# Kernel tuning notes

Hardware: AMD Instinct MI355X
Metric: run time of the kernel (lower is better)

## Reference

```python
import jax, jax.numpy as jnp
import numpy as np

HIDDEN = 1024
N_HEADS = 16
N_KV = 4
HEAD_DIM = HIDDEN // N_HEADS  # 64


def setup_inputs() -> dict:
    key = jax.random.key(0)
    ks = jax.random.split(key, 10)
    B, S, D = 2, 2048, HIDDEN
    s = 0.02
    return {
        "hidden_states": jax.random.normal(ks[0], (B, S, D), jnp.float32),
        "attention_mask": jnp.ones((B, S), jnp.float32),
        "Wq": jax.random.normal(ks[1], (D, N_HEADS * HEAD_DIM), jnp.float32) * s,
        "bq": jnp.zeros((N_HEADS * HEAD_DIM,), jnp.float32),
        "Wk": jax.random.normal(ks[2], (D, N_KV * HEAD_DIM), jnp.float32) * s,
        "bk": jnp.zeros((N_KV * HEAD_DIM,), jnp.float32),
        "Wv": jax.random.normal(ks[3], (D, N_KV * HEAD_DIM), jnp.float32) * s,
        "bv": jnp.zeros((N_KV * HEAD_DIM,), jnp.float32),
        "Wo": jax.random.normal(ks[4], (D, D), jnp.float32) * s,
        "bo": jnp.zeros((D,), jnp.float32),
    }


def _rope(x):
    # x: [B, H, S, Dh]; half-split RoPE as in the torch module
    S, Dh = x.shape[-2], x.shape[-1]
    inv_freq = 1.0 / (10000.0 ** (jnp.arange(0, Dh, 2, dtype=jnp.float32) / Dh))
    freqs = jnp.arange(S, dtype=jnp.float32)[:, None] * inv_freq[None, :]  # [S, Dh/2]
    cos, sin = jnp.cos(freqs), jnp.sin(freqs)
    x1, x2 = jnp.split(x, 2, axis=-1)
    return jnp.concatenate([x1 * cos - x2 * sin, x1 * sin + x2 * cos], axis=-1)


def reference(hidden_states, attention_mask, Wq, bq, Wk, bk, Wv, bv, Wo, bo):
    B, S, D = hidden_states.shape
    q = (hidden_states @ Wq + bq).reshape(B, S, N_HEADS, HEAD_DIM).transpose(0, 2, 1, 3)
    k = (hidden_states @ Wk + bk).reshape(B, S, N_KV, HEAD_DIM).transpose(0, 2, 1, 3)
    v = (hidden_states @ Wv + bv).reshape(B, S, N_KV, HEAD_DIM).transpose(0, 2, 1, 3)
    q = _rope(q)
    k = _rope(k)
    rep = N_HEADS // N_KV
    k = jnp.repeat(k, rep, axis=1)  # [B, H, S, Dh]
    v = jnp.repeat(v, rep, axis=1)
    bias = (1.0 - attention_mask[:, None, None, :]) * -1e9  # [B,1,1,S]
    scores = jnp.einsum("bhqd,bhkd->bhqk", q, k) / jnp.sqrt(jnp.float32(HEAD_DIM))
    attn = jax.nn.softmax(scores + bias, axis=-1)
    out = jnp.einsum("bhqk,bhkd->bhqd", attn, v)
    out = out.transpose(0, 2, 1, 3).reshape(B, S, D)
    return out @ Wo + bo
```

## Files before the change

kernel.cpp:

```cpp
#include <hip/hip_runtime.h>

typedef __bf16 bf16;
typedef __attribute__((ext_vector_type(8))) __bf16 bf16x8;
typedef __attribute__((ext_vector_type(4))) __bf16 bf16x4;
typedef __attribute__((ext_vector_type(4))) float f32x4;
typedef __attribute__((ext_vector_type(16))) float f32x16;
typedef __attribute__((ext_vector_type(4))) unsigned int uint4v;

#define LOG2E 1.44269504088896340736f
#define QSCALE 0.18033688011112042f

__device__ inline void tr_tile(const float* __restrict__ in, bf16* __restrict__ out,
                               int R, int C, int bx, int by, int tid) {
    __shared__ float t[32][33];
    int tx = tid & 31, ty = tid >> 5;
    int rbase = by * 32, cbase = bx * 32;
#pragma unroll
    for (int i = 0; i < 4; i++) {
        int r = ty + i * 8;
        t[r][tx] = in[(size_t)(rbase + r) * C + cbase + tx];
    }
    __syncthreads();
#pragma unroll
    for (int i = 0; i < 4; i++) {
        int r = ty + i * 8;
        out[(size_t)(cbase + r) * R + rbase + tx] = (bf16)t[tx][r];
    }
}

__global__ __launch_bounds__(256) void prep_k(const float* __restrict__ X,
                                              const float* __restrict__ Wq,
                                              const float* __restrict__ Wk,
                                              const float* __restrict__ Wv,
                                              const float* __restrict__ Wo,
                                              const float* __restrict__ mask,
                                              bf16* __restrict__ Xb,
                                              bf16* __restrict__ WqT,
                                              bf16* __restrict__ WkT,
                                              bf16* __restrict__ WvT,
                                              bf16* __restrict__ WoT,
                                              float2* __restrict__ rt,
                                              float* __restrict__ Mb,
                                              int* __restrict__ mflags) {
    int blk = blockIdx.x, tid = threadIdx.x;
    if (blk < 2048) {
        int idx = (blk * 256 + tid) * 8;
        float4 a = *(const float4*)(X + idx);
        float4 b = *(const float4*)(X + idx + 4);
        bf16 v[8] = {(bf16)a.x, (bf16)a.y, (bf16)a.z, (bf16)a.w,
                     (bf16)b.x, (bf16)b.y, (bf16)b.z, (bf16)b.w};
        *(uint4*)(Xb + idx) = *(const uint4*)v;
    } else if (blk < 3072) {
        int t = blk - 2048; tr_tile(Wq, WqT, 1024, 1024, t & 31, t >> 5, tid);
    } else if (blk < 3328) {
        int t = blk - 3072; tr_tile(Wk, WkT, 1024, 256, t & 7, t >> 3, tid);
    } else if (blk < 3584) {
        int t = blk - 3328; tr_tile(Wv, WvT, 1024, 256, t & 7, t >> 3, tid);
    } else if (blk < 4608) {
        int t = blk - 3584; tr_tile(Wo, WoT, 1024, 1024, t & 31, t >> 5, tid);
    } else if (blk < 4864) {
        int idx = (blk - 4608) * 256 + tid;
        int s = idx >> 5, i = idx & 31;
        float inv = exp2f(-0.41524100370589830f * (float)i);
        float ang = (float)s * inv;
        rt[idx] = make_float2(cosf(ang), sinf(ang));
    } else {
        __shared__ int sflag;
        int b = blk - 4864;
        if (tid == 0) sflag = 1;
        __syncthreads();
        const float* mrow = mask + (size_t)b * 2048;
        int i0 = tid * 8;
        bool ones = true;
#pragma unroll
        for (int j = 0; j < 8; j++) {
            float m = mrow[i0 + j];
            if (m != 1.0f) ones = false;
            Mb[(size_t)b * 2048 + i0 + j] = (1.0f - m) * (-1e9f) * LOG2E;
        }
        if (!ones) sflag = 0;
        __syncthreads();
        if (tid == 0) mflags[b] = sflag;
    }
}

__device__ __forceinline__ void gemm_main_db(bf16* __restrict__ pool,
                                             const bf16* __restrict__ A,
                                             const bf16* __restrict__ BT,
                                             int m0, int n0, int tid,
                                             f32x4 (&acc)[2][4]) {
    int w = tid >> 6, lane = tid & 63, l15 = lane & 15, quad = lane >> 4;

    int srow = lane >> 3;
    int kx = ((lane & 7) ^ srow) * 8;
    const bf16* ga0 = A + (size_t)(m0 + w * 32 + srow) * 1024 + kx;
    const bf16* gb0 = BT + (size_t)(n0 + w * 16 + srow) * 1024 + kx;
    int laofs = (w * 32) * 64 + lane * 8;
    int lbofs = 128 * 64 + (w * 16) * 64 + lane * 8;

#define GSTAGE(K0, BUF)                                                                             \
    do {                                                                                            \
        bf16* gbase = pool + (BUF) * 12288;                                                         \
        _Pragma("unroll")                                                                           \
        for (int p = 0; p < 4; p++)                                                                 \
            __builtin_amdgcn_global_load_lds(                                                       \
                (const __attribute__((address_space(1))) unsigned int*)(ga0 + (size_t)p * 8 * 1024 + (K0)), \
                (__attribute__((address_space(3))) unsigned int*)(gbase + laofs + p * 512), 16, 0, 0); \
        _Pragma("unroll")                                                                           \
        for (int p = 0; p < 2; p++)                                                                 \
            __builtin_amdgcn_global_load_lds(                                                       \
                (const __attribute__((address_space(1))) unsigned int*)(gb0 + (size_t)p * 8 * 1024 + (K0)), \
                (__attribute__((address_space(3))) unsigned int*)(gbase + lbofs + p * 512), 16, 0, 0); \
    } while (0)

    GSTAGE(0, 0);
    __syncthreads();

    for (int ks = 0; ks < 16; ks++) {
        int cb = ks & 1;
        if (ks < 15) GSTAGE((ks + 1) * 64, cb ^ 1);
        const bf16* As = pool + cb * 12288;
        const bf16* Bs = As + 128 * 64;
#pragma unroll
        for (int half = 0; half < 2; half++) {
            bf16x8 a[2], bfr[4];
            int kp = ((half * 4 + quad) ^ (l15 & 7)) * 8;
#pragma unroll
            for (int i = 0; i < 2; i++)
                a[i] = *(const bf16x8*)&As[(w * 32 + i * 16 + l15) * 64 + kp];
#pragma unroll
            for (int j = 0; j < 4; j++)
                bfr[j] = *(const bf16x8*)&Bs[(j * 16 + l15) * 64 + kp];
#pragma unroll
            for (int i = 0; i < 2; i++)
#pragma unroll
                for (int j = 0; j < 4; j++)
                    acc[i][j] = __builtin_amdgcn_mfma_f32_16x16x32_bf16(a[i], bfr[j], acc[i][j], 0, 0, 0);
        }
        __syncthreads();
    }
#undef GSTAGE
}

__global__ __launch_bounds__(256) void qkv_gemm2(const bf16* __restrict__ Xb,
                                                 const bf16* __restrict__ WTall,
                                                 const float* __restrict__ bq,
                                                 const float* __restrict__ bk,
                                                 const float* __restrict__ bv,
                                                 const float2* __restrict__ rt,
                                                 bf16* __restrict__ Qb,
                                                 bf16* __restrict__ Kb,
                                                 bf16* __restrict__ VbT) {
    __shared__ __align__(16) bf16 pool[2 * 12288];
    int tt = blockIdx.x, gy = blockIdx.y, tid = threadIdx.x;
    f32x4 acc[2][4] = {};
    gemm_main_db(pool, Xb, WTall, tt * 128, gy * 64, tid, acc);

    int w = tid >> 6, lane = tid & 63, l15 = lane & 15, quad = lane >> 4;

    if (gy >= 20) {
        int kvh = gy - 20;
        const float* bias = bv + kvh * 64;
        bf16* T = pool;
#pragma unroll
        for (int i = 0; i < 2; i++)
#pragma unroll
            for (int r = 0; r < 4; r++) {
                int s_local = w * 32 + i * 16 + quad * 4 + r;
#pragma unroll
                for (int j = 0; j < 4; j++) {
                    int d = j * 16 + l15;
                    T[d * 136 + s_local] = (bf16)(acc[i][j][r] + bias[d]);
                }
            }
        __syncthreads();
        int d = tid & 63, sblk = tid >> 6;
        int b = tt >> 4, s_base = (tt & 15) * 128 + sblk * 32;
        const bf16* Trow = T + d * 136 + sblk * 32;
        size_t orow = ((size_t)(b * 4 + kvh) * 64 + d) * 2048 + s_base;
#pragma unroll
        for (int c = 0; c < 4; c++)
            *(uint4*)(VbT + orow + c * 8) = *(const uint4*)(Trow + c * 8);
        return;
    }

    const float* bias;
    bf16* dst;
    int mode, head;
    if (gy < 16) { head = gy;      bias = bq + head * 64; dst = Qb; mode = 0; }
    else         { head = gy - 16; bias = bk + head * 64; dst = Kb; mode = 1; }

#pragma unroll
    for (int i = 0; i < 2; i++) {
#pragma unroll
        for (int r = 0; r < 4; r++) {
            int token = tt * 128 + w * 32 + i * 16 + quad * 4 + r;
            int b = token >> 11, s = token & 2047;
            float vals[4];
#pragma unroll
            for (int j = 0; j < 4; j++) vals[j] = acc[i][j][r] + bias[j * 16 + l15];
#pragma unroll
            for (int c = 0; c < 2; c++) {
                float2 cs2 = rt[s * 32 + c * 16 + l15];
                float x1 = vals[c], x2 = vals[c + 2];
                vals[c]     = x1 * cs2.x - x2 * cs2.y;
                vals[c + 2] = x1 * cs2.y + x2 * cs2.x;
            }
            if (mode == 0) {
#pragma unroll
                for (int j = 0; j < 4; j++) vals[j] *= QSCALE;
            }
            size_t base;
            if (mode == 0) base = (((size_t)b * 16 + head) * 2048 + s) * 64;
            else           base = (((size_t)b * 4  + head) * 2048 + s) * 64;
#pragma unroll
            for (int j = 0; j < 4; j++) dst[base + j * 16 + l15] = (bf16)vals[j];
        }
    }
}

__global__ __launch_bounds__(256) void oproj_gemm2(const bf16* __restrict__ Ab,
                                                   const bf16* __restrict__ WoT,
                                                   const float* __restrict__ bo,
                                                   float* __restrict__ out) {
    __shared__ __align__(16) bf16 pool[2 * 12288];
    int tt = blockIdx.x, nt = blockIdx.y, tid = threadIdx.x;
    f32x4 acc[2][4] = {};
    gemm_main_db(pool, Ab, WoT, tt * 128, nt * 64, tid, acc);

    int w = tid >> 6, lane = tid & 63, l15 = lane & 15, quad = lane >> 4;
#pragma unroll
    for (int i = 0; i < 2; i++) {
#pragma unroll
        for (int r = 0; r < 4; r++) {
            int token = tt * 128 + w * 32 + i * 16 + quad * 4 + r;
#pragma unroll
            for (int j = 0; j < 4; j++) {
                int n = nt * 64 + j * 16 + l15;
                out[(size_t)token * 1024 + n] = acc[i][j][r] + bo[n];
            }
        }
    }
}

__global__ __launch_bounds__(256, 4) void attn_k(const bf16* __restrict__ Qb,
                                                 const bf16* __restrict__ Kb,
                                                 const bf16* __restrict__ VbT,
                                                 const float* __restrict__ Mb,
                                                 const int* __restrict__ mflags,
                                                 bf16* __restrict__ Opb,
                                                 float* __restrict__ Lp) {
    int qt = blockIdx.x, h = blockIdx.y, z = blockIdx.z;
    int b = z >> 1, sp = z & 1;
    int kvh = h >> 2;
    int kt0 = sp * 16;

    __shared__ bf16 Ks[2][64 * 64];
    __shared__ bf16 Vs[2][64 * 64];

    int tid = threadIdx.x, w = tid >> 6, lane = tid & 63, l31 = lane & 31, hi = lane >> 5;

    const bool maskOnes = (mflags[b] != 0);

    bf16x8 qa[4];
    {
        size_t qrow = (((size_t)b * 16 + h) * 2048 + (size_t)qt * 128 + w * 32 + l31) * 64;
#pragma unroll
        for (int ds = 0; ds < 4; ds++)
            qa[ds] = *(const bf16x8*)(Qb + qrow + ds * 16 + hi * 8);
    }

    f32x16 oacc[2] = {};
    float lsum = 0.f;

    size_t kRow = ((size_t)b * 4 + kvh) * 2048;
    size_t vRow = ((size_t)b * 4 + kvh) * 64;

    int srow = lane >> 3;
    int kx = ((lane & 7) ^ srow) * 8;
    const bf16* gk0 = Kb + (kRow + w * 16 + srow) * 64 + kx;
    const bf16* gv0 = VbT + (vRow + w * 16 + srow) * 2048 + kx;
    int lofs = (w * 16) * 64 + lane * 8;

#define STAGE(KT, BUF)                                                                              \
    do {                                                                                            \
        _Pragma("unroll")                                                                           \
        for (int p = 0; p < 2; p++) {                                                               \
            __builtin_amdgcn_global_load_lds(                                                       \
                (const __attribute__((address_space(1))) unsigned int*)(gk0 + ((size_t)(KT) * 64 + p * 8) * 64), \
                (__attribute__((address_space(3))) unsigned int*)(&Ks[BUF][0] + lofs + p * 512), 16, 0, 0); \
            __builtin_amdgcn_global_load_lds(                                                       \
                (const __attribute__((address_space(1))) unsigned int*)(gv0 + (size_t)p * 8 * 2048 + (KT) * 64), \
                (__attribute__((address_space(3))) unsigned int*)(&Vs[BUF][0] + lofs + p * 512), 16, 0, 0); \
        }                                                                                           \
    } while (0)

    STAGE(kt0, 0);
    __syncthreads();

    const float* mbase = Mb + (size_t)b * 2048 + hi * 4;

    for (int kt = 0; kt < 16; kt++) {
        int cb = kt & 1;
        if (kt < 15) STAGE(kt0 + kt + 1, cb ^ 1);
        int ktg = kt0 + kt;

        const bf16* ksb = &Ks[cb][0];
        const bf16* vsb = &Vs[cb][0];

        uint4v paw[4];
#pragma unroll
        for (int kh = 0; kh < 2; kh++) {
            bf16x8 ka[4];
#pragma unroll
            for (int ds = 0; ds < 4; ds++) {
                int gran = ((ds * 2 + hi) ^ (l31 & 7)) * 8;
                ka[ds] = *(const bf16x8*)&ksb[(kh * 32 + l31) * 64 + gran];
            }
            f32x16 s = {};
#pragma unroll
            for (int ds = 0; ds < 4; ds++)
                s = __builtin_amdgcn_mfma_f32_32x32x16_bf16(ka[ds], qa[ds], s, 0, 0, 0);
            if (!maskOnes) {
#pragma unroll
                for (int g = 0; g < 4; g++) {
                    f32x4 b4 = *(const f32x4*)(mbase + ktg * 64 + kh * 32 + g * 8);
#pragma unroll
                    for (int r = 0; r < 4; r++) s[g * 4 + r] += b4[r];
                }
            }
#pragma unroll
            for (int i = 0; i < 16; i++) { s[i] = exp2f(s[i]); lsum += s[i]; }
            unsigned int d0, d1, d2, d3, d4, d5, d6, d7;
            asm("v_cvt_pk_bf16_f32 %0, %1, %2" : "=v"(d0) : "v"(s[0]),  "v"(s[1]));
            asm("v_cvt_pk_bf16_f32 %0, %1, %2" : "=v"(d1) : "v"(s[2]),  "v"(s[3]));
            asm("v_cvt_pk_bf16_f32 %0, %1, %2" : "=v"(d2) : "v"(s[4]),  "v"(s[5]));
            asm("v_cvt_pk_bf16_f32 %0, %1, %2" : "=v"(d3) : "v"(s[6]),  "v"(s[7]));
            asm("v_cvt_pk_bf16_f32 %0, %1, %2" : "=v"(d4) : "v"(s[8]),  "v"(s[9]));
            asm("v_cvt_pk_bf16_f32 %0, %1, %2" : "=v"(d5) : "v"(s[10]), "v"(s[11]));
            asm("v_cvt_pk_bf16_f32 %0, %1, %2" : "=v"(d6) : "v"(s[12]), "v"(s[13]));
            asm("v_cvt_pk_bf16_f32 %0, %1, %2" : "=v"(d7) : "v"(s[14]), "v"(s[15]));
            asm("v_permlane32_swap_b32 %0, %1" : "+v"(d0), "+v"(d2));
            asm("v_permlane32_swap_b32 %0, %1" : "+v"(d1), "+v"(d3));
            asm("v_permlane32_swap_b32 %0, %1" : "+v"(d4), "+v"(d6));
            asm("v_permlane32_swap_b32 %0, %1" : "+v"(d5), "+v"(d7));
            paw[kh * 2 + 0][0] = d0; paw[kh * 2 + 0][1] = d1;
            paw[kh * 2 + 0][2] = d2; paw[kh * 2 + 0][3] = d3;
            paw[kh * 2 + 1][0] = d4; paw[kh * 2 + 1][1] = d5;
            paw[kh * 2 + 1][2] = d6; paw[kh * 2 + 1][3] = d7;
        }

#pragma unroll
        for (int dg = 0; dg < 2; dg++)
#pragma unroll
            for (int ks = 0; ks < 4; ks++) {
                int gran = ((ks * 2 + hi) ^ (l31 & 7)) * 8;
                bf16x8 vb = *(const bf16x8*)&vsb[(dg * 32 + l31) * 64 + gran];
                oacc[dg] = __builtin_amdgcn_mfma_f32_32x32x16_bf16(
                    __builtin_bit_cast(bf16x8, paw[ks]), vb, oacc[dg], 0, 0, 0);
            }
        __syncthreads();
    }
#undef STAGE

    lsum += __shfl_xor(lsum, 32, 64);

#pragma unroll
    for (int dg = 0; dg < 2; dg++)
#pragma unroll
        for (int reg = 0; reg < 16; reg++) {
            int q = qt * 128 + w * 32 + (reg & 3) + 8 * (reg >> 2) + 4 * hi;
            Opb[((size_t)sp * 4096 + (size_t)b * 2048 + q) * 1024 + h * 64 + dg * 32 + l31] =
                (bf16)oacc[dg][reg];
        }
    if (hi == 0)
        Lp[((size_t)(sp * 2 + b) * 16 + h) * 2048 + qt * 128 + w * 32 + l31] = lsum;
}

__global__ __launch_bounds__(256) void merge_k(const bf16* __restrict__ Opb,
                                               const float* __restrict__ Lp,
                                               bf16* __restrict__ Ab) {
    int idx = (blockIdx.x * 256 + threadIdx.x) * 8;
    int tok = idx >> 10;
    int col = idx & 1023;
    int h = col >> 6;
    int b = tok >> 11, q = tok & 2047;
    float l0 = Lp[((size_t)b * 16 + h) * 2048 + q];
    float l1 = Lp[((size_t)(2 + b) * 16 + h) * 2048 + q];
    float inv = 1.0f / (l0 + l1);
    bf16x8 a = *(const bf16x8*)(Opb + idx);
    bf16x8 c = *(const bf16x8*)(Opb + (size_t)4096 * 1024 + idx);
    bf16 o[8];
#pragma unroll
    for (int j = 0; j < 8; j++) o[j] = (bf16)(((float)a[j] + (float)c[j]) * inv);
    *(uint4*)(Ab + idx) = *(const uint4*)o;
}

extern "C" void kernel_launch(void* const* d_in, const int* in_sizes, int n_in,
                              void* d_out, int out_size, void* d_ws, size_t ws_size,
                              hipStream_t stream) {
    const float* X    = (const float*)d_in[0];
    const float* mask = (const float*)d_in[1];
    const float* Wq   = (const float*)d_in[2];
    const float* bq   = (const float*)d_in[3];
    const float* Wk   = (const float*)d_in[4];
    const float* bk   = (const float*)d_in[5];
    const float* Wv   = (const float*)d_in[6];
    const float* bv   = (const float*)d_in[7];
    const float* Wo   = (const float*)d_in[8];
    const float* bo   = (const float*)d_in[9];
    float* out = (float*)d_out;
    bf16* ws  = (bf16*)d_ws;

    bf16* Xb  = ws;
    bf16* WqT = Xb + (size_t)4096 * 1024;
    bf16* WkT = WqT + 1024 * 1024;
    bf16* WvT = WkT + 256 * 1024;
    bf16* WoT = WvT + 256 * 1024;
    bf16* Qb  = WoT + 1024 * 1024;
    bf16* Kb  = Qb + (size_t)2 * 16 * 2048 * 64;
    bf16* VbT = Kb + (size_t)2 * 4 * 2048 * 64;
    bf16* Ab  = VbT + (size_t)2 * 4 * 2048 * 64;
    float2* rt = (float2*)(Ab + (size_t)2 * 2048 * 1024);
    float* Mb  = (float*)(rt + 2048 * 32);
    int* mflags = (int*)(Mb + 2 * 2048);
    bf16* Opb = (bf16*)(mflags + 4);
    float* Lp = (float*)(Opb + (size_t)2 * 4096 * 1024);

    prep_k<<<4866, 256, 0, stream>>>(X, Wq, Wk, Wv, Wo, mask, Xb, WqT, WkT, WvT, WoT, rt, Mb, mflags);
    qkv_gemm2<<<dim3(32, 24), 256, 0, stream>>>(Xb, WqT, bq, bk, bv, rt, Qb, Kb, VbT);
    attn_k<<<dim3(16, 16, 4), 256, 0, stream>>>(Qb, Kb, VbT, Mb, mflags, Opb, Lp);
    merge_k<<<2048, 256, 0, stream>>>(Opb, Lp, Ab);
    oproj_gemm2<<<dim3(32, 16), 256, 0, stream>>>(Ab, WoT, bo, out);
}
```

Measured before the change: 180.6 us.

## Fuse split-KV merge into output projection GEMM A-tile loading

```diff
diff --git a/kernel.cpp b/kernel.cpp
--- a/kernel.cpp
+++ b/kernel.cpp
@@ -219,16 +219,107 @@
     }
 }
 
-__global__ __launch_bounds__(256) void oproj_gemm2(const bf16* __restrict__ Ab,
+__global__ __launch_bounds__(256) void oproj_gemm2(const bf16* __restrict__ Opb,
+                                                   const float* __restrict__ Lp,
                                                    const bf16* __restrict__ WoT,
                                                    const float* __restrict__ bo,
                                                    float* __restrict__ out) {
     __shared__ __align__(16) bf16 pool[2 * 12288];
     int tt = blockIdx.x, nt = blockIdx.y, tid = threadIdx.x;
+    int w = tid >> 6, lane = tid & 63, l15 = lane & 15, quad = lane >> 4;
+    int srow = lane >> 3;
+    int kx = ((lane & 7) ^ srow) * 8;
+
+    const bf16* gb0 = WoT + (size_t)(nt * 64 + w * 16 + srow) * 1024 + kx;
+    int laofs = (w * 32) * 64 + lane * 8;
+    int lbofs = 128 * 64 + (w * 16) * 64 + lane * 8;
+
+    int m0 = tt * 128;
+    int bb = m0 >> 11;
+    size_t arow[4];
+    int qq[4];
+#pragma unroll
+    for (int p = 0; p < 4; p++) {
+        int t = m0 + w * 32 + srow + p * 8;
+        arow[p] = (size_t)t * 1024 + kx;
+        qq[p] = t & 2047;
+    }
+    const bf16* slab1 = Opb + (size_t)4096 * 1024;
+    const float* lpA = Lp + (size_t)bb * 16 * 2048;
+    const float* lpB = Lp + (size_t)(2 + bb) * 16 * 2048;
+
+    bf16x8 ra0[4], ra1[4];
+    float lp0[4], lp1[4];
+
+#define OISSUE_A(KS)                                                         \
+    do {                                                                     \
+        _Pragma("unroll")                                                    \
+        for (int p = 0; p < 4; p++) {                                        \
+            ra0[p] = *(const bf16x8*)(Opb + arow[p] + (KS) * 64);            \
+            ra1[p] = *(const bf16x8*)(slab1 + arow[p] + (KS) * 64);          \
+            lp0[p] = lpA[(size_t)(KS) * 2048 + qq[p]];                       \
+            lp1[p] = lpB[(size_t)(KS) * 2048 + qq[p]];                       \
+        }                                                                    \
+    } while (0)
+
+#define OWRITE_A(BUF)                                                        \
+    do {                                                                     \
+        bf16* gbase = pool + (BUF) * 12288;                                  \
+        _Pragma("unroll")                                                    \
+        for (int p = 0; p < 4; p++) {                                        \
+            float inv = 1.0f / (lp0[p] + lp1[p]);                            \
+            bf16 o[8];                                                       \
+            _Pragma("unroll")                                                \
+            for (int e = 0; e < 8; e++)                                      \
+                o[e] = (bf16)(((float)ra0[p][e] + (float)ra1[p][e]) * inv);  \
+            *(uint4*)(gbase + laofs + p * 512) = *(const uint4*)o;           \
+        }                                                                    \
+    } while (0)
+
+#define OISSUE_B(KS, BUF)                                                    \
+    do {                                                                     \
+        bf16* gbase = pool + (BUF) * 12288;                                  \
+        _Pragma("unroll")                                                    \
+        for (int p = 0; p < 2; p++)                                          \
+            __builtin_amdgcn_global_load_lds(                                \
+                (const __attribute__((address_space(1))) unsigned int*)(gb0 + (size_t)p * 8 * 1024 + (KS) * 64), \
+                (__attribute__((address_space(3))) unsigned int*)(gbase + lbofs + p * 512), 16, 0, 0); \
+    } while (0)
+
+    OISSUE_A(0);
+    OISSUE_B(0, 0);
+    OWRITE_A(0);
+    __syncthreads();
+
     f32x4 acc[2][4] = {};
-    gemm_main_db(pool, Ab, WoT, tt * 128, nt * 64, tid, acc);
-
-    int w = tid >> 6, lane = tid & 63, l15 = lane & 15, quad = lane >> 4;
+    for (int ks = 0; ks < 16; ks++) {
+        int cb = ks & 1;
+        if (ks < 15) { OISSUE_A(ks + 1); OISSUE_B(ks + 1, cb ^ 1); }
+        const bf16* As = pool + cb * 12288;
+        const bf16* Bs = As + 128 * 64;
+#pragma unroll
+        for (int half = 0; half < 2; half++) {
+            bf16x8 a[2], bfr[4];
+            int kp = ((half * 4 + quad) ^ (l15 & 7)) * 8;
+#pragma unroll
+            for (int i = 0; i < 2; i++)
+                a[i] = *(const bf16x8*)&As[(w * 32 + i * 16 + l15) * 64 + kp];
+#pragma unroll
+            for (int j = 0; j < 4; j++)
+                bfr[j] = *(const bf16x8*)&Bs[(j * 16 + l15) * 64 + kp];
+#pragma unroll
+            for (int i = 0; i < 2; i++)
+#pragma unroll
+                for (int j = 0; j < 4; j++)
+                    acc[i][j] = __builtin_amdgcn_mfma_f32_16x16x32_bf16(a[i], bfr[j], acc[i][j], 0, 0, 0);
+        }
+        if (ks < 15) OWRITE_A(cb ^ 1);
+        __syncthreads();
+    }
+#undef OISSUE_A
+#undef OWRITE_A
+#undef OISSUE_B
+
 #pragma unroll
     for (int i = 0; i < 2; i++) {
 #pragma unroll
@@ -377,25 +468,6 @@
         Lp[((size_t)(sp * 2 + b) * 16 + h) * 2048 + qt * 128 + w * 32 + l31] = lsum;
 }
 
-__global__ __launch_bounds__(256) void merge_k(const bf16* __restrict__ Opb,
-                                               const float* __restrict__ Lp,
-                                               bf16* __restrict__ Ab) {
-    int idx = (blockIdx.x * 256 + threadIdx.x) * 8;
-    int tok = idx >> 10;
-    int col = idx & 1023;
-    int h = col >> 6;
-    int b = tok >> 11, q = tok & 2047;
-    float l0 = Lp[((size_t)b * 16 + h) * 2048 + q];
-    float l1 = Lp[((size_t)(2 + b) * 16 + h) * 2048 + q];
-    float inv = 1.0f / (l0 + l1);
-    bf16x8 a = *(const bf16x8*)(Opb + idx);
-    bf16x8 c = *(const bf16x8*)(Opb + (size_t)4096 * 1024 + idx);
-    bf16 o[8];
-#pragma unroll
-    for (int j = 0; j < 8; j++) o[j] = (bf16)(((float)a[j] + (float)c[j]) * inv);
-    *(uint4*)(Ab + idx) = *(const uint4*)o;
-}
-
 extern "C" void kernel_launch(void* const* d_in, const int* in_sizes, int n_in,
                               void* d_out, int out_size, void* d_ws, size_t ws_size,
                               hipStream_t stream) {
@@ -430,6 +502,5 @@
     prep_k<<<4866, 256, 0, stream>>>(X, Wq, Wk, Wv, Wo, mask, Xb, WqT, WkT, WvT, WoT, rt, Mb, mflags);
     qkv_gemm2<<<dim3(32, 24), 256, 0, stream>>>(Xb, WqT, bq, bk, bv, rt, Qb, Kb, VbT);
     attn_k<<<dim3(16, 16, 4), 256, 0, stream>>>(Qb, Kb, VbT, Mb, mflags, Opb, Lp);
-    merge_k<<<2048, 256, 0, stream>>>(Opb, Lp, Ab);
-    oproj_gemm2<<<dim3(32, 16), 256, 0, stream>>>(Ab, WoT, bo, out);
-}
+    oproj_gemm2<<<dim3(32, 16), 256, 0, stream>>>(Opb, Lp, WoT, bo, out);
+}
```

After: 188.8 us. +4.5%, slower.
